# Performance work log

Measured on AMD Instinct MI355X. Metric: run time of the kernel, lower is better.

The kernel has to match this reference:

```python
import jax, jax.numpy as jnp
import numpy as np
from jax import lax

B, N, T, D, H = 8, 64, 128, 256, 8
DK = D // H
K_SIZE = 3
SCALE = 1.0 / np.sqrt(DK)
NEG = -1e9


def conv1d_same(x, w, b):
    # x: (M, Cin, T), w: (Cout, Cin, K) torch Conv1d layout, padding='same'
    y = lax.conv_general_dilated(x, w, window_strides=(1,), padding='SAME',
                                 dimension_numbers=('NCH', 'OIH', 'NCH'))
    return y + b[None, :, None]


def setup_inputs() -> dict:
    rng = jax.random.key(0)
    ks = jax.random.split(rng, 12)
    s = 0.05
    return {
        'query': jax.random.normal(ks[0], (B, N, T, D), jnp.float32),
        'key': jax.random.normal(ks[1], (B, N, T, D), jnp.float32),
        'value': jax.random.normal(ks[2], (B, N, T, D), jnp.float32),
        'key_padding_mask': jax.random.randint(ks[3], (B, N, T), 0, 2).astype(jnp.bool_),
        'attn_mask': jax.random.randint(ks[4], (T, T), 0, 2).astype(jnp.int32),
        'conv_q_w': jax.random.normal(ks[5], (D, D, K_SIZE), jnp.float32) * s,
        'conv_q_b': jnp.zeros((D,), jnp.float32),
        'conv_k_w': jax.random.normal(ks[6], (D, D, K_SIZE), jnp.float32) * s,
        'conv_k_b': jnp.zeros((D,), jnp.float32),
        'v_w': jax.random.normal(ks[7], (D, D), jnp.float32) * s,  # torch Linear: (out, in)
        'v_b': jnp.zeros((D,), jnp.float32),
        'out_w': jax.random.normal(ks[8], (D, D), jnp.float32) * s,
        'out_b': jnp.zeros((D,), jnp.float32),
    }


def reference(query, key, value, key_padding_mask, attn_mask,
              conv_q_w, conv_q_b, conv_k_w, conv_k_b, v_w, v_b, out_w, out_b):
    Bq, Nq, Tq, Dq = query.shape
    Tk = key.shape[2]
    # Conv1d Q/K projections ('same' padding, mode='1d')
    q_in = query.reshape(Bq * Nq, Tq, Dq).transpose(0, 2, 1)  # (BN, D, Tq)
    k_in = key.reshape(Bq * Nq, Tk, Dq).transpose(0, 2, 1)
    q = conv1d_same(q_in, conv_q_w, conv_q_b).transpose(0, 2, 1)  # (BN, Tq, D)
    k = conv1d_same(k_in, conv_k_w, conv_k_b).transpose(0, 2, 1)
    Q = q.reshape(Bq, Nq, Tq, H, DK).transpose(0, 1, 3, 2, 4)  # (B,N,H,Tq,dk)
    Kh = k.reshape(Bq, Nq, Tk, H, DK).transpose(0, 1, 3, 2, 4)
    V = (jnp.einsum('bntd,ed->bnte', value, v_w) + v_b)
    V = V.reshape(Bq, Nq, Tk, H, DK).transpose(0, 1, 3, 2, 4)  # (B,N,H,Tk,dk)
    scores = jnp.einsum('bnhqd,bnhkd->bnhqk', Q, Kh) * SCALE
    scores = jnp.where(key_padding_mask[:, :, None, None, :], NEG, scores)
    scores = jnp.where(attn_mask[None, None, None, :, :] == 0, NEG, scores)
    attn = jax.nn.softmax(scores, axis=-1)
    x = jnp.einsum('bnhqk,bnhkd->bnhqd', attn, V)
    x = x.transpose(0, 1, 3, 2, 4).reshape(Bq, Nq, Tq, Dq)
    return jnp.einsum('bntd,ed->bnte', x, out_w) + out_b
```

## Files before the change

### kernel.cpp

```cpp
#include <hip/hip_runtime.h>

#define TT 128
#define DD 256
#define NH 8
#define HD 32
#define SCALEF 0.17677669529663687f
#define NEGV -1e9f

typedef short bf16x8 __attribute__((ext_vector_type(8)));
typedef float f32x4 __attribute__((ext_vector_type(4)));

__device__ inline unsigned short f2bf(float f) {
    unsigned u = __float_as_uint(f);
    unsigned r = (u + 0x7FFFu + ((u >> 16) & 1u)) >> 16;
    return (unsigned short)r;
}
__device__ inline unsigned pk2(float a, float b) {
    return (unsigned)f2bf(a) | ((unsigned)f2bf(b) << 16);
}

__global__ void cvt_weights_kernel(
    const float* __restrict__ wq, const float* __restrict__ wk,
    const float* __restrict__ vw, const float* __restrict__ ow,
    const unsigned char* __restrict__ kpm8,
    unsigned short* __restrict__ wqf, unsigned short* __restrict__ wkf,
    unsigned short* __restrict__ vwf, unsigned short* __restrict__ owf,
    int* __restrict__ flagp)
{
    if (blockIdx.x == 1280) {
        __shared__ int f;
        if (threadIdx.x == 0) f = 0;
        __syncthreads();
        bool loc = false;
        for (int i = threadIdx.x; i < 4096; i += 256)
            if ((i & 3) && kpm8[i]) loc = true;
        if (loc) f = 1;
        __syncthreads();
        if (threadIdx.x == 0) *flagp = f;
        return;
    }
    int t = blockIdx.x * 256 + threadIdx.x;
    if (t < 196608) {
        int f = t >> 9, r = t & 511, l = r >> 3, s = r & 7;
        int k = f >> 7, jr = (f >> 3) & 15, c32 = f & 7;
        int j = jr * 16 + (l & 15);
        int ci = c32 * 32 + (l >> 4) * 8 + s;
        int src = j * 768 + ci * 3 + k;
        wqf[t] = f2bf(wq[src]);
        wkf[t] = f2bf(wk[src]);
    } else {
        int o = t - 196608;
        int oo = o & 65535;
        int f = oo >> 9, r = oo & 511, l = r >> 3, s = r & 7;
        int er = f >> 3, c32 = f & 7;
        int e = er * 16 + (l & 15);
        int d = c32 * 32 + (l >> 4) * 8 + s;
        if (o < 65536) vwf[oo] = f2bf(vw[e * 256 + d]);
        else           owf[oo] = f2bf(ow[e * 256 + d]);
    }
}

#define XP 264

__global__ __launch_bounds__(512, 4) void proj_kernel(
    const float* __restrict__ query, const float* __restrict__ key,
    const float* __restrict__ value,
    const unsigned short* __restrict__ wqf, const unsigned short* __restrict__ wkf,
    const unsigned short* __restrict__ vwf,
    const float* __restrict__ bq, const float* __restrict__ bk,
    const float* __restrict__ vbias,
    short* __restrict__ qkb, short* __restrict__ vbuf)
{
    __shared__ __align__(16) short Xs[130 * XP];

    const int tid = threadIdx.x;
    const int bn = blockIdx.x, which = blockIdx.y;
    const int lane = tid & 63, wv = tid >> 6;
    const int lr = lane & 15, rg = lane >> 4, k8 = rg * 8;

    const float* __restrict__ X =
        (which == 0 ? query : which == 1 ? key : value) + (size_t)bn * TT * DD;

    if (which < 2) {
        const unsigned short* __restrict__ W = which ? wkf : wqf;
        const float* __restrict__ bias = which ? bk : bq;
        const int j0 = (wv & 3) * 64;
        const int t0 = (wv >> 2) * 64;

        for (int i = tid; i < 130 * 64; i += 512) {
            int row = i >> 6, c4 = i & 63, g = row - 1;
            float4 x4 = make_float4(0.f, 0.f, 0.f, 0.f);
            if (g >= 0 && g < TT)
                x4 = *(const float4*)(X + g * DD + c4 * 4);
            uint2 p; p.x = pk2(x4.x, x4.y); p.y = pk2(x4.z, x4.w);
            *(uint2*)&Xs[row * XP + c4 * 4] = p;
        }
        __syncthreads();

        f32x4 acc[4][4];
        #pragma unroll
        for (int mf = 0; mf < 4; ++mf)
            #pragma unroll
            for (int r = 0; r < 4; ++r) {
                float bv = bias[j0 + mf * 16 + rg * 4 + r];
                #pragma unroll
                for (int nf = 0; nf < 4; ++nf) acc[mf][nf][r] = bv;
            }

        #pragma unroll
        for (int k = 0; k < 3; ++k) {
            #pragma unroll
            for (int c32 = 0; c32 < 8; ++c32) {
                bf16x8 aa[4];
                #pragma unroll
                for (int mf = 0; mf < 4; ++mf)
                    aa[mf] = *(const bf16x8*)(W +
                        ((((k * 16 + (j0 >> 4) + mf) * 8 + c32) << 9)
                         + lane * 8));
                bf16x8 bb[4];
                #pragma unroll
                for (int nf = 0; nf < 4; ++nf)
                    bb[nf] = *(const bf16x8*)&Xs[(t0 + nf * 16 + lr + k) * XP
                                                 + c32 * 32 + k8];
                #pragma unroll
                for (int mf = 0; mf < 4; ++mf)
                    #pragma unroll
                    for (int nf = 0; nf < 4; ++nf)
                        acc[mf][nf] = __builtin_amdgcn_mfma_f32_16x16x32_bf16(
                            aa[mf], bb[nf], acc[mf][nf], 0, 0, 0);
            }
        }
        short* cell = qkb + (size_t)bn * 65536 + which * 32768;
        #pragma unroll
        for (int mf = 0; mf < 4; ++mf)
            #pragma unroll
            for (int nf = 0; nf < 4; ++nf) {
                int fr = ((t0 >> 4) + nf) * 8 + (j0 >> 5) + (mf >> 1);
                int off = (fr << 9) + (lr + 16 * ((mf & 1) * 2 + (rg >> 1))) * 8
                          + (rg & 1) * 4;
                uint2 p;
                p.x = pk2(acc[mf][nf][0], acc[mf][nf][1]);
                p.y = pk2(acc[mf][nf][2], acc[mf][nf][3]);
                *(uint2*)&cell[off] = p;
            }
    } else {
        const int e0 = (wv & 3) * 64;
        const int t0 = (wv >> 2) * 64;

        for (int i = tid; i < 128 * 64; i += 512) {
            int row = i >> 6, c4 = i & 63;
            float4 x4 = *(const float4*)(X + row * DD + c4 * 4);
            uint2 p; p.x = pk2(x4.x, x4.y); p.y = pk2(x4.z, x4.w);
            *(uint2*)&Xs[row * XP + c4 * 4] = p;
        }
        __syncthreads();

        f32x4 acc4[4][4];
        #pragma unroll
        for (int nf = 0; nf < 4; ++nf) {
            float bv = vbias[e0 + nf * 16 + lr];
            #pragma unroll
            for (int mf = 0; mf < 4; ++mf)
                #pragma unroll
                for (int r = 0; r < 4; ++r) acc4[mf][nf][r] = bv;
        }

        #pragma unroll
        for (int c32 = 0; c32 < 8; ++c32) {
            bf16x8 aa[4];
            #pragma unroll
            for (int mf = 0; mf < 4; ++mf)
                aa[mf] = *(const bf16x8*)&Xs[(t0 + mf * 16 + lr) * XP
                                             + c32 * 32 + k8];
            bf16x8 bb[4];
            #pragma unroll
            for (int nf = 0; nf < 4; ++nf)
                bb[nf] = *(const bf16x8*)(vwf +
                    (((((e0 >> 4) + nf) * 8 + c32) << 9) + lane * 8));
            #pragma unroll
            for (int mf = 0; mf < 4; ++mf)
                #pragma unroll
                for (int nf = 0; nf < 4; ++nf)
                    acc4[mf][nf] = __builtin_amdgcn_mfma_f32_16x16x32_bf16(
                        aa[mf], bb[nf], acc4[mf][nf], 0, 0, 0);
        }
        short* vcell = vbuf + (size_t)bn * 32768;
        #pragma unroll
        for (int mf = 0; mf < 4; ++mf)
            #pragma unroll
            for (int nf = 0; nf < 4; ++nf) {
                int fr = (((e0 >> 4) + nf) << 2) + (t0 >> 5) + (mf >> 1);
                int off = (fr << 9) + (lr + 16 * ((mf & 1) * 2 + (rg >> 1))) * 8
                          + (rg & 1) * 4;
                uint2 p;
                p.x = pk2(acc4[mf][nf][0], acc4[mf][nf][1]);
                p.y = pk2(acc4[mf][nf][2], acc4[mf][nf][3]);
                *(uint2*)&vcell[off] = p;
            }
    }
}

__global__ __launch_bounds__(512, 2) void attn_out_fused(
    short* qkb, const short* __restrict__ vbuf,
    const unsigned short* __restrict__ owf, const float* __restrict__ ob,
    const unsigned char* __restrict__ kpm8, const int* __restrict__ kpm32,
    const int* __restrict__ amask, const int* __restrict__ flagp)
{
    __shared__ __align__(16) short Ps[8 * 32 * 136];
    __shared__ __align__(16) short xs[128 * XP];
    __shared__ unsigned char maskb[2048];

    const int tid = threadIdx.x;
    const int bid = blockIdx.x;
    const int bn = (bid & 7) * 64 + (bid >> 3);
    const int lane = tid & 63, wv = tid >> 6;
    const int lr = lane & 15, rg = lane >> 4, k8 = rg * 8;
    const bool kpm_u8 = (*flagp != 0);

    {
        const unsigned char* kp8 = kpm8 + (size_t)bn * TT;
        const int* kp32 = kpm32 + (size_t)bn * TT;
        for (int i = tid; i < 2048; i += 512) {
            int row = i >> 4, c = i & 15;
            unsigned m = 0;
            #pragma unroll
            for (int nf = 0; nf < 8; ++nf) {
                int col = c + nf * 16;
                int kdead = kpm_u8 ? (int)kp8[col] : kp32[col];
                int adead = (amask[row * TT + col] == 0) ? 1 : 0;
                m |= (unsigned)(((kdead != 0) ? 1 : 0) | adead) << nf;
            }
            maskb[i] = (unsigned char)m;
        }
    }

    const short* qcell = qkb + (size_t)bn * 65536;
    const short* kcell = qcell + 32768;
    const short* vcell = vbuf + (size_t)bn * 32768;

    bf16x8 kb[8];
    #pragma unroll
    for (int nf = 0; nf < 8; ++nf)
        kb[nf] = *(const bf16x8*)(kcell + (((nf * 8 + wv) << 9) + lane * 8));

    __syncthreads();

    short* Pw = Ps + wv * 32 * 136;

    #pragma unroll
    for (int mtp = 0; mtp < 4; ++mtp) {
        bf16x8 qa[2];
        #pragma unroll
        for (int mf = 0; mf < 2; ++mf)
            qa[mf] = *(const bf16x8*)(qcell +
                ((((mtp * 2 + mf) * 8 + wv) << 9) + lane * 8));

        f32x4 sc[2][8];
        #pragma unroll
        for (int nf = 0; nf < 8; ++nf) {
            f32x4 z = { 0.f, 0.f, 0.f, 0.f };
            sc[0][nf] = __builtin_amdgcn_mfma_f32_16x16x32_bf16(qa[0], kb[nf], z, 0, 0, 0);
            sc[1][nf] = __builtin_amdgcn_mfma_f32_16x16x32_bf16(qa[1], kb[nf], z, 0, 0, 0);
        }

        float linv[2][4];
        #pragma unroll
        for (int mf = 0; mf < 2; ++mf)
            #pragma unroll
            for (int r = 0; r < 4; ++r) {
                int row = mtp * 32 + mf * 16 + rg * 4 + r;
                unsigned mb = maskb[row * 16 + lr];
                float v[8];
                float vmax = -3.4e38f;
                #pragma unroll
                for (int nf = 0; nf < 8; ++nf) {
                    float t = sc[mf][nf][r] * SCALEF;
                    if ((mb >> nf) & 1) t = NEGV;
                    v[nf] = t;
                    vmax = fmaxf(vmax, t);
                }
                #pragma unroll
                for (int d = 1; d < 16; d <<= 1)
                    vmax = fmaxf(vmax, __shfl_xor(vmax, d, 64));
                float ls = 0.f;
                #pragma unroll
                for (int nf = 0; nf < 8; ++nf) {
                    float p = __expf(v[nf] - vmax);
                    ls += p;
                    sc[mf][nf][r] = p;
                }
                #pragma unroll
                for (int d = 1; d < 16; d <<= 1)
                    ls += __shfl_xor(ls, d, 64);
                linv[mf][r] = 1.f / ls;
            }

        #pragma unroll
        for (int mf = 0; mf < 2; ++mf)
            #pragma unroll
            for (int r = 0; r < 4; ++r) {
                int q = mf * 16 + rg * 4 + r;
                #pragma unroll
                for (int nf = 0; nf < 8; ++nf)
                    Pw[q * 136 + nf * 16 + lr] = (short)f2bf(sc[mf][nf][r]);
            }

        f32x4 xacc[2][2];
        {
            f32x4 z = { 0.f, 0.f, 0.f, 0.f };
            xacc[0][0] = z; xacc[0][1] = z; xacc[1][0] = z; xacc[1][1] = z;
        }
        #pragma unroll
        for (int kk = 0; kk < 4; ++kk) {
            bf16x8 pa0 = *(const bf16x8*)&Pw[lr * 136 + kk * 32 + k8];
            bf16x8 pa1 = *(const bf16x8*)&Pw[(16 + lr) * 136 + kk * 32 + k8];
            bf16x8 vb0 = *(const bf16x8*)(vcell + ((((wv * 2 + 0) * 4 + kk) << 9) + lane * 8));
            bf16x8 vb1 = *(const bf16x8*)(vcell + ((((wv * 2 + 1) * 4 + kk) << 9) + lane * 8));
            xacc[0][0] = __builtin_amdgcn_mfma_f32_16x16x32_bf16(pa0, vb0, xacc[0][0], 0, 0, 0);
            xacc[0][1] = __builtin_amdgcn_mfma_f32_16x16x32_bf16(pa0, vb1, xacc[0][1], 0, 0, 0);
            xacc[1][0] = __builtin_amdgcn_mfma_f32_16x16x32_bf16(pa1, vb0, xacc[1][0], 0, 0, 0);
            xacc[1][1] = __builtin_amdgcn_mfma_f32_16x16x32_bf16(pa1, vb1, xacc[1][1], 0, 0, 0);
        }

        #pragma unroll
        for (int mf = 0; mf < 2; ++mf)
            #pragma unroll
            for (int nf = 0; nf < 2; ++nf)
                #pragma unroll
                for (int r = 0; r < 4; ++r) {
                    int t = mtp * 32 + mf * 16 + rg * 4 + r;
                    xs[t * XP + wv * HD + nf * 16 + lr] =
                        (short)f2bf(xacc[mf][nf][r] * linv[mf][r]);
                }
    }

    __syncthreads();

    f32x4 acc[16];
    {
        f32x4 z = { 0.f, 0.f, 0.f, 0.f };
        #pragma unroll
        for (int nf = 0; nf < 16; ++nf) acc[nf] = z;
    }
    #pragma unroll
    for (int dc = 0; dc < 8; ++dc) {
        bf16x8 aa = *(const bf16x8*)&xs[(wv * 16 + lr) * XP + dc * 32 + k8];
        #pragma unroll
        for (int nf = 0; nf < 16; ++nf) {
            bf16x8 bb = *(const bf16x8*)(owf + (((nf * 8 + dc) << 9) + lane * 8));
            acc[nf] = __builtin_amdgcn_mfma_f32_16x16x32_bf16(aa, bb, acc[nf], 0, 0, 0);
        }
    }

    float* fcell = (float*)qkb + (size_t)bn * 32768;
    #pragma unroll
    for (int nf = 0; nf < 16; ++nf) {
        float bb = ob[nf * 16 + lr];
        #pragma unroll
        for (int r = 0; r < 4; ++r)
            fcell[(wv * 16 + rg * 4 + r) * DD + nf * 16 + lr] = acc[nf][r] + bb;
    }
}

extern "C" void kernel_launch(void* const* d_in, const int* in_sizes, int n_in,
                              void* d_out, int out_size, void* d_ws, size_t ws_size,
                              hipStream_t stream) {
    (void)in_sizes; (void)n_in; (void)out_size; (void)ws_size;
    const float* query = (const float*)d_in[0];
    const float* key   = (const float*)d_in[1];
    const float* value = (const float*)d_in[2];
    const void*  kpm   = d_in[3];
    const int*   amask = (const int*)d_in[4];
    const float* wq = (const float*)d_in[5];
    const float* bq = (const float*)d_in[6];
    const float* wk = (const float*)d_in[7];
    const float* bk = (const float*)d_in[8];
    const float* vw = (const float*)d_in[9];
    const float* vb = (const float*)d_in[10];
    const float* ow = (const float*)d_in[11];
    const float* ob = (const float*)d_in[12];

    short* qkb = (short*)d_out;
    unsigned short* wqf = (unsigned short*)d_ws;
    unsigned short* wkf = wqf + 196608;
    unsigned short* vwf = wkf + 196608;
    unsigned short* owf = vwf + 65536;
    int* flagp = (int*)((short*)d_ws + 524288);
    short* vbuf = (short*)d_ws + 524296;

    cvt_weights_kernel<<<dim3(1281), dim3(256), 0, stream>>>(
        wq, wk, vw, ow, (const unsigned char*)kpm, wqf, wkf, vwf, owf, flagp);

    proj_kernel<<<dim3(512, 3), dim3(512), 0, stream>>>(
        query, key, value, wqf, wkf, vwf, bq, bk, vb, qkb, vbuf);

    attn_out_fused<<<dim3(512), dim3(512), 0, stream>>>(
        qkb, vbuf, owf, ob, (const unsigned char*)kpm, (const int*)kpm,
        amask, flagp);
}
```

Baseline: 169.7 us.

## Split projection K dimension into two halves and prefetch second half during MFMA

The projection kernel now stages the input row block in two channel halves. The first half goes to LDS, and the second half's global loads are issued into registers before the first half's MFMA loop runs, so memory latency overlaps compute. The held-in-register prefetch (8-9 float4 per thread) raises register pressure under launch_bounds(512,4) and adds a second barrier. LDS footprint stays about the same (two half-width buffers instead of one full-width).

```diff
diff --git a/kernel.cpp b/kernel.cpp
--- a/kernel.cpp
+++ b/kernel.cpp
@@ -60,7 +60,7 @@
     }
 }
 
-#define XP 264
+#define HP 136
 
 __global__ __launch_bounds__(512, 4) void proj_kernel(
     const float* __restrict__ query, const float* __restrict__ key,
@@ -71,7 +71,8 @@
     const float* __restrict__ vbias,
     short* __restrict__ qkb, short* __restrict__ vbuf)
 {
-    __shared__ __align__(16) short Xs[130 * XP];
+    __shared__ __align__(16) short Xs0[130 * HP];
+    __shared__ __align__(16) short Xs1[130 * HP];
 
     const int tid = threadIdx.x;
     const int bn = blockIdx.x, which = blockIdx.y;
@@ -86,16 +87,30 @@
         const float* __restrict__ bias = which ? bk : bq;
         const int j0 = (wv & 3) * 64;
         const int t0 = (wv >> 2) * 64;
-
-        for (int i = tid; i < 130 * 64; i += 512) {
-            int row = i >> 6, c4 = i & 63, g = row - 1;
+        const int jr0 = j0 >> 4;
+
+        for (int i = tid; i < 130 * 32; i += 512) {
+            int row = i >> 5, c4 = i & 31, g = row - 1;
             float4 x4 = make_float4(0.f, 0.f, 0.f, 0.f);
             if (g >= 0 && g < TT)
                 x4 = *(const float4*)(X + g * DD + c4 * 4);
             uint2 p; p.x = pk2(x4.x, x4.y); p.y = pk2(x4.z, x4.w);
-            *(uint2*)&Xs[row * XP + c4 * 4] = p;
-        }
-        __syncthreads();
+            *(uint2*)&Xs0[row * HP + c4 * 4] = p;
+        }
+        __syncthreads();
+
+        float4 xn[9];
+        #pragma unroll
+        for (int u = 0; u < 9; ++u) {
+            int i = tid + u * 512;
+            float4 v = make_float4(0.f, 0.f, 0.f, 0.f);
+            if (i < 130 * 32) {
+                int row = i >> 5, c4 = i & 31, g = row - 1;
+                if (g >= 0 && g < TT)
+                    v = *(const float4*)(X + g * DD + 128 + c4 * 4);
+            }
+            xn[u] = v;
+        }
 
         f32x4 acc[4][4];
         #pragma unroll
@@ -110,18 +125,18 @@
         #pragma unroll
         for (int k = 0; k < 3; ++k) {
             #pragma unroll
-            for (int c32 = 0; c32 < 8; ++c32) {
+            for (int cl = 0; cl < 4; ++cl) {
+                const int c32 = cl;
                 bf16x8 aa[4];
                 #pragma unroll
                 for (int mf = 0; mf < 4; ++mf)
                     aa[mf] = *(const bf16x8*)(W +
-                        ((((k * 16 + (j0 >> 4) + mf) * 8 + c32) << 9)
-                         + lane * 8));
+                        ((((k * 16 + jr0 + mf) * 8 + c32) << 9) + lane * 8));
                 bf16x8 bb[4];
                 #pragma unroll
                 for (int nf = 0; nf < 4; ++nf)
-                    bb[nf] = *(const bf16x8*)&Xs[(t0 + nf * 16 + lr + k) * XP
-                                                 + c32 * 32 + k8];
+                    bb[nf] = *(const bf16x8*)&Xs0[(t0 + nf * 16 + lr + k) * HP
+                                                  + cl * 32 + k8];
                 #pragma unroll
                 for (int mf = 0; mf < 4; ++mf)
                     #pragma unroll
@@ -130,6 +145,42 @@
                             aa[mf], bb[nf], acc[mf][nf], 0, 0, 0);
             }
         }
+
+        #pragma unroll
+        for (int u = 0; u < 9; ++u) {
+            int i = tid + u * 512;
+            if (i < 130 * 32) {
+                int row = i >> 5, c4 = i & 31;
+                uint2 p; p.x = pk2(xn[u].x, xn[u].y); p.y = pk2(xn[u].z, xn[u].w);
+                *(uint2*)&Xs1[row * HP + c4 * 4] = p;
+            }
+        }
+        __syncthreads();
+
+        #pragma unroll
+        for (int k = 0; k < 3; ++k) {
+            #pragma unroll
+            for (int cl = 0; cl < 4; ++cl) {
+                const int c32 = 4 + cl;
+                bf16x8 aa[4];
+                #pragma unroll
+                for (int mf = 0; mf < 4; ++mf)
+                    aa[mf] = *(const bf16x8*)(W +
+                        ((((k * 16 + jr0 + mf) * 8 + c32) << 9) + lane * 8));
+                bf16x8 bb[4];
+                #pragma unroll
+                for (int nf = 0; nf < 4; ++nf)
+                    bb[nf] = *(const bf16x8*)&Xs1[(t0 + nf * 16 + lr + k) * HP
+                                                  + cl * 32 + k8];
+                #pragma unroll
+                for (int mf = 0; mf < 4; ++mf)
+                    #pragma unroll
+                    for (int nf = 0; nf < 4; ++nf)
+                        acc[mf][nf] = __builtin_amdgcn_mfma_f32_16x16x32_bf16(
+                            aa[mf], bb[nf], acc[mf][nf], 0, 0, 0);
+            }
+        }
+
         short* cell = qkb + (size_t)bn * 65536 + which * 32768;
         #pragma unroll
         for (int mf = 0; mf < 4; ++mf)
@@ -146,14 +197,23 @@
     } else {
         const int e0 = (wv & 3) * 64;
         const int t0 = (wv >> 2) * 64;
-
-        for (int i = tid; i < 128 * 64; i += 512) {
-            int row = i >> 6, c4 = i & 63;
+        const int er0 = e0 >> 4;
+
+        for (int i = tid; i < 128 * 32; i += 512) {
+            int row = i >> 5, c4 = i & 31;
             float4 x4 = *(const float4*)(X + row * DD + c4 * 4);
             uint2 p; p.x = pk2(x4.x, x4.y); p.y = pk2(x4.z, x4.w);
-            *(uint2*)&Xs[row * XP + c4 * 4] = p;
-        }
-        __syncthreads();
+            *(uint2*)&Xs0[row * HP + c4 * 4] = p;
+        }
+        __syncthreads();
+
+        float4 xn[8];
+        #pragma unroll
+        for (int u = 0; u < 8; ++u) {
+            int i = tid + u * 512;
+            int row = i >> 5, c4 = i & 31;
+            xn[u] = *(const float4*)(X + row * DD + 128 + c4 * 4);
+        }
 
         f32x4 acc4[4][4];
         #pragma unroll
@@ -166,17 +226,18 @@
         }
 
         #pragma unroll
-        for (int c32 = 0; c32 < 8; ++c32) {
+        for (int cl = 0; cl < 4; ++cl) {
+            const int c32 = cl;
             bf16x8 aa[4];
             #pragma unroll
             for (int mf = 0; mf < 4; ++mf)
-                aa[mf] = *(const bf16x8*)&Xs[(t0 + mf * 16 + lr) * XP
-                                             + c32 * 32 + k8];
+                aa[mf] = *(const bf16x8*)&Xs0[(t0 + mf * 16 + lr) * HP
+                                              + cl * 32 + k8];
             bf16x8 bb[4];
             #pragma unroll
             for (int nf = 0; nf < 4; ++nf)
                 bb[nf] = *(const bf16x8*)(vwf +
-                    (((((e0 >> 4) + nf) * 8 + c32) << 9) + lane * 8));
+                    ((((er0 + nf) * 8 + c32) << 9) + lane * 8));
             #pragma unroll
             for (int mf = 0; mf < 4; ++mf)
                 #pragma unroll
@@ -184,12 +245,43 @@
                     acc4[mf][nf] = __builtin_amdgcn_mfma_f32_16x16x32_bf16(
                         aa[mf], bb[nf], acc4[mf][nf], 0, 0, 0);
         }
+
+        #pragma unroll
+        for (int u = 0; u < 8; ++u) {
+            int i = tid + u * 512;
+            int row = i >> 5, c4 = i & 31;
+            uint2 p; p.x = pk2(xn[u].x, xn[u].y); p.y = pk2(xn[u].z, xn[u].w);
+            *(uint2*)&Xs1[row * HP + c4 * 4] = p;
+        }
+        __syncthreads();
+
+        #pragma unroll
+        for (int cl = 0; cl < 4; ++cl) {
+            const int c32 = 4 + cl;
+            bf16x8 aa[4];
+            #pragma unroll
+            for (int mf = 0; mf < 4; ++mf)
+                aa[mf] = *(const bf16x8*)&Xs1[(t0 + mf * 16 + lr) * HP
+                                              + cl * 32 + k8];
+            bf16x8 bb[4];
+            #pragma unroll
+            for (int nf = 0; nf < 4; ++nf)
+                bb[nf] = *(const bf16x8*)(vwf +
+                    ((((er0 + nf) * 8 + c32) << 9) + lane * 8));
+            #pragma unroll
+            for (int mf = 0; mf < 4; ++mf)
+                #pragma unroll
+                for (int nf = 0; nf < 4; ++nf)
+                    acc4[mf][nf] = __builtin_amdgcn_mfma_f32_16x16x32_bf16(
+                        aa[mf], bb[nf], acc4[mf][nf], 0, 0, 0);
+        }
+
         short* vcell = vbuf + (size_t)bn * 32768;
         #pragma unroll
         for (int mf = 0; mf < 4; ++mf)
             #pragma unroll
             for (int nf = 0; nf < 4; ++nf) {
-                int fr = (((e0 >> 4) + nf) << 2) + (t0 >> 5) + (mf >> 1);
+                int fr = ((er0 + nf) << 2) + (t0 >> 5) + (mf >> 1);
                 int off = (fr << 9) + (lr + 16 * ((mf & 1) * 2 + (rg >> 1))) * 8
                           + (rg & 1) * 4;
                 uint2 p;
@@ -199,6 +291,8 @@
             }
     }
 }
+
+#define XP 264
 
 __global__ __launch_bounds__(512, 2) void attn_out_fused(
     short* qkb, const short* __restrict__ vbuf,
```

Measured after the change: 205.7 us. +21.2%, slower.
